# Kernel optimization log

Hardware: AMD Instinct MI355X
Metric: run time of the kernel (lower is better)

## Reference

```python
import jax, jax.numpy as jnp
import numpy as np

TOP_K = 8


def setup_inputs() -> dict:
    key = jax.random.key(0)
    k1, k2 = jax.random.split(key)
    N, D, E = 16384, 4096, 64
    x = jax.random.normal(k1, (N, D), dtype=jnp.float32)
    W = jax.random.normal(k2, (E, D), dtype=jnp.float32) * (1.0 / np.sqrt(D))
    b = jnp.zeros((E,), dtype=jnp.float32)
    return {"x": x, "W": W, "b": b}


def reference(x, W, b):
    # gate: [N, E]
    logits = jnp.einsum('nd,ed->ne', x, W) + b
    top_vals, top_idx = jax.lax.top_k(logits, TOP_K)  # [N, k]
    N = logits.shape[0]
    rows = jnp.arange(N)[:, None]  # [N, 1] broadcast against [N, k]
    neg_inf = jnp.full_like(logits, -jnp.inf)
    sparse = neg_inf.at[rows, top_idx].set(top_vals)
    sparse_logits = jax.nn.softmax(sparse, axis=-1)  # non-topk entries -> 0
    return (sparse_logits, top_idx)
```

## Files before the change

### kernel.cpp

```cpp
#include <hip/hip_runtime.h>
#include <cfloat>
#include <cmath>

#define M     16384
#define K     4096
#define E     64
#define TOPK  8
#define GAP_THRESH 1e-4f

#define SPLIT 4
#define KPS   (K / SPLIT)
#define NCH   (KPS / 32)

typedef __attribute__((ext_vector_type(8))) short bf16x8;
typedef __attribute__((ext_vector_type(4))) float f32x4;


__device__ __forceinline__ short f2bf(float f) {
    unsigned u = __builtin_bit_cast(unsigned, f);
    u += 0x7FFFu + ((u >> 16) & 1u);
    return (short)(u >> 16);
}
__device__ __forceinline__ float bf2f(short h) {
    unsigned u = ((unsigned)(unsigned short)h) << 16;
    return __builtin_bit_cast(float, u);
}

__global__ __launch_bounds__(256) void prep_kernel(const float* __restrict__ W,
                                                   short* __restrict__ Whf,
                                                   short* __restrict__ Wlf,
                                                   int* __restrict__ count) {
    int t = blockIdx.x * 256 + threadIdx.x;
    float w = W[t];
    short h = f2bf(w);
    short lo = f2bf(w - bf2f(h));
    int e = t >> 12, k = t & 4095;
    int gc = k >> 5, kk = k & 31;
    size_t fidx = (((size_t)gc * 4 + (e >> 4)) * 64 + (kk >> 3) * 16 + (e & 15)) * 8
                  + (kk & 7);
    Whf[fidx] = h;
    Wlf[fidx] = lo;
    if (t == 0) *count = 0;
}

struct XW {
    float4 xa, xb;
    bf16x8 h0, h1, h2, h3, l0, l1, l2, l3;
};

__device__ __forceinline__ void load_set(XW& s, const float* gx,
                                         const short* ph, const short* pl, int cc) {
    const int ko = cc * 32;
    s.xa = *reinterpret_cast<const float4*>(gx + ko);
    s.xb = *reinterpret_cast<const float4*>(gx + ko + 4);
    const short* bh = ph + (size_t)cc * 2048;
    const short* bl = pl + (size_t)cc * 2048;
    s.h0 = *reinterpret_cast<const bf16x8*>(bh);
    s.h1 = *reinterpret_cast<const bf16x8*>(bh + 512);
    s.h2 = *reinterpret_cast<const bf16x8*>(bh + 1024);
    s.h3 = *reinterpret_cast<const bf16x8*>(bh + 1536);
    s.l0 = *reinterpret_cast<const bf16x8*>(bl);
    s.l1 = *reinterpret_cast<const bf16x8*>(bl + 512);
    s.l2 = *reinterpret_cast<const bf16x8*>(bl + 1024);
    s.l3 = *reinterpret_cast<const bf16x8*>(bl + 1536);
}

__device__ __forceinline__ void compute_set(const XW& s, f32x4 acc[4]) {
    float vv[8] = {s.xa.x, s.xa.y, s.xa.z, s.xa.w, s.xb.x, s.xb.y, s.xb.z, s.xb.w};
    bf16x8 ah, al;
#pragma unroll
    for (int j = 0; j < 8; ++j) {
        short hh = f2bf(vv[j]);
        ah[j] = hh;
        al[j] = f2bf(vv[j] - bf2f(hh));
    }
    acc[0] = __builtin_amdgcn_mfma_f32_16x16x32_bf16(ah, s.h0, acc[0], 0, 0, 0);
    acc[0] = __builtin_amdgcn_mfma_f32_16x16x32_bf16(ah, s.l0, acc[0], 0, 0, 0);
    acc[0] = __builtin_amdgcn_mfma_f32_16x16x32_bf16(al, s.h0, acc[0], 0, 0, 0);
    acc[1] = __builtin_amdgcn_mfma_f32_16x16x32_bf16(ah, s.h1, acc[1], 0, 0, 0);
    acc[1] = __builtin_amdgcn_mfma_f32_16x16x32_bf16(ah, s.l1, acc[1], 0, 0, 0);
    acc[1] = __builtin_amdgcn_mfma_f32_16x16x32_bf16(al, s.h1, acc[1], 0, 0, 0);
    acc[2] = __builtin_amdgcn_mfma_f32_16x16x32_bf16(ah, s.h2, acc[2], 0, 0, 0);
    acc[2] = __builtin_amdgcn_mfma_f32_16x16x32_bf16(ah, s.l2, acc[2], 0, 0, 0);
    acc[2] = __builtin_amdgcn_mfma_f32_16x16x32_bf16(al, s.h2, acc[2], 0, 0, 0);
    acc[3] = __builtin_amdgcn_mfma_f32_16x16x32_bf16(ah, s.h3, acc[3], 0, 0, 0);
    acc[3] = __builtin_amdgcn_mfma_f32_16x16x32_bf16(ah, s.l3, acc[3], 0, 0, 0);
    acc[3] = __builtin_amdgcn_mfma_f32_16x16x32_bf16(al, s.h3, acc[3], 0, 0, 0);
}

__global__ __launch_bounds__(256) void gate_kernel(
    const float* __restrict__ x,
    const short* __restrict__ Whf,
    const short* __restrict__ Wlf,
    float* __restrict__ part)
{
    const int t  = threadIdx.x;
    const int l  = t & 63;
    const int wv = t >> 6;
    const int h    = blockIdx.x & (SPLIT - 1);
    const int row0 = (blockIdx.x >> 2) * 64 + wv * 16;
    const int k0   = h * KPS;

    const int kg   = l >> 4;
    const int xrow = row0 + (l & 15);

    const float* gx = x + (size_t)xrow * K + k0 + kg * 8;
    const short* ph = Whf + ((size_t)(k0 >> 5) * 4) * 512 + (size_t)l * 8;
    const short* pl = Wlf + ((size_t)(k0 >> 5) * 4) * 512 + (size_t)l * 8;

    f32x4 acc[4] = {{0,0,0,0},{0,0,0,0},{0,0,0,0},{0,0,0,0}};

    XW A, B;
    load_set(A, gx, ph, pl, 0);
    for (int c = 0; c < NCH; c += 2) {
        load_set(B, gx, ph, pl, c + 1);
        compute_set(A, acc);
        if (c + 2 < NCH) load_set(A, gx, ph, pl, c + 2);
        compute_set(B, acc);
    }

#pragma unroll
    for (int et = 0; et < 4; ++et)
#pragma unroll
        for (int r = 0; r < 4; ++r)
            part[((size_t)h * M + row0 + (l >> 4) * 4 + r) * E + et * 16 + (l & 15)]
                = acc[et][r];
}

__global__ __launch_bounds__(256) void reduce_kernel(
    const float* __restrict__ part,
    const float* __restrict__ b,
    float* __restrict__ outp,
    float* __restrict__ outi,
    int*   __restrict__ count,
    int*   __restrict__ list)
{
    const int lane = threadIdx.x & 63;
    const int w    = threadIdx.x >> 6;
    const int row  = blockIdx.x * 4 + w;

    float orig = b[lane];
#pragma unroll
    for (int hh = 0; hh < SPLIT; ++hh)
        orig += part[((size_t)hh * M + row) * E + lane];

    float cur = orig;
    float vals[9];
    float myidxf = 0.0f;
    bool  sel = false;

#pragma unroll
    for (int i = 0; i < 9; ++i) {
        float m = cur;
#pragma unroll
        for (int off = 32; off > 0; off >>= 1)
            m = fmaxf(m, __shfl_xor(m, off, 64));
        unsigned long long msk = __ballot(cur == m);
        int il = __ffsll((long long)msk) - 1;
        vals[i] = m;
        if (lane == il) { cur = -FLT_MAX; if (i < TOPK) sel = true; }
        if (i < TOPK && lane == i) myidxf = (float)il;
    }

    float ssum = 0.0f;
#pragma unroll
    for (int i = 0; i < TOPK; ++i) ssum += expf(vals[i] - vals[0]);
    float p = sel ? (expf(orig - vals[0]) / ssum) : 0.0f;

    outp[(size_t)row * E + lane] = p;
    if (lane < TOPK) outi[(size_t)row * TOPK + lane] = myidxf;

    float mingap = FLT_MAX;
#pragma unroll
    for (int i = 0; i < 8; ++i) mingap = fminf(mingap, vals[i] - vals[i + 1]);
    if (lane == 0 && mingap < GAP_THRESH) {
        int pos = atomicAdd(count, 1);
        if (pos < M) list[pos] = row;
    }
}

__global__ __launch_bounds__(512) void fix_kernel(
    const float* __restrict__ x,
    const float* __restrict__ W,
    const float* __restrict__ b,
    float* __restrict__ outp,
    float* __restrict__ outi,
    const int* __restrict__ count,
    const int* __restrict__ list)
{
    __shared__ float  xs[K];
    __shared__ double lsum[E];
    const int t   = threadIdx.x;
    const int l   = t & 63;
    const int wv  = t >> 6;
    const int cnt = *count;

    for (int i = blockIdx.x; i < cnt; i += gridDim.x) {
        const int row = list[i];

        const float4* xr4 = reinterpret_cast<const float4*>(x + (size_t)row * K);
        reinterpret_cast<float4*>(xs)[t]       = xr4[t];
        reinterpret_cast<float4*>(xs)[512 + t] = xr4[512 + t];
        __syncthreads();

        const int e0 = wv * 8;
        double acc[8] = {};
#pragma unroll 4
        for (int j = 0; j < 16; ++j) {
            float4 xv = reinterpret_cast<const float4*>(xs)[l + 64 * j];
#pragma unroll
            for (int e8 = 0; e8 < 8; ++e8) {
                float4 wv4 = reinterpret_cast<const float4*>(
                    W + (size_t)(e0 + e8) * K)[l + 64 * j];
                acc[e8] = fma((double)xv.x, (double)wv4.x, acc[e8]);
                acc[e8] = fma((double)xv.y, (double)wv4.y, acc[e8]);
                acc[e8] = fma((double)xv.z, (double)wv4.z, acc[e8]);
                acc[e8] = fma((double)xv.w, (double)wv4.w, acc[e8]);
            }
        }

#pragma unroll
        for (int e8 = 0; e8 < 8; ++e8) {
            double v = acc[e8];
#pragma unroll
            for (int off = 32; off > 0; off >>= 1)
                v += __shfl_xor(v, off, 64);
            if (l == e8) lsum[e0 + e8] = v;
        }
        __syncthreads();

        if (wv == 0) {
            const double orig = lsum[l] + (double)b[l];
            double cur = orig;

            double vals[TOPK];
            float  myidxf = 0.0f;
            bool   sel = false;

#pragma unroll
            for (int tt = 0; tt < TOPK; ++tt) {
                double m = cur;
#pragma unroll
                for (int off = 32; off > 0; off >>= 1) {
                    double o = __shfl_xor(m, off, 64);
                    m = fmax(m, o);
                }
                unsigned long long msk = __ballot(cur == m);
                int il = __ffsll((long long)msk) - 1;
                vals[tt] = m;
                if (l == il) { cur = -DBL_MAX; sel = true; }
                if (l == tt)  myidxf = (float)il;
            }

            double ssum = 0.0;
#pragma unroll
            for (int tt = 0; tt < TOPK; ++tt) ssum += exp(vals[tt] - vals[0]);
            float p = sel ? (float)(exp(orig - vals[0]) / ssum) : 0.0f;

            outp[(size_t)row * E + l] = p;
            if (l < TOPK) outi[(size_t)row * TOPK + l] = myidxf;
        }
        __syncthreads();
    }
}

__global__ __launch_bounds__(64) void fallback_kernel(
    const float* __restrict__ x,
    const float* __restrict__ W,
    const float* __restrict__ b,
    float* __restrict__ outp,
    float* __restrict__ outi)
{
    const int row = blockIdx.x * 64 + threadIdx.x;
    double lg[64];
#pragma unroll
    for (int e = 0; e < 64; ++e) lg[e] = (double)b[e];
    const float* xr = x + (size_t)row * K;
    for (int k = 0; k < K; k += 4) {
        float4 xa = *reinterpret_cast<const float4*>(xr + k);
        double xd[4] = {(double)xa.x, (double)xa.y, (double)xa.z, (double)xa.w};
#pragma unroll
        for (int e = 0; e < 64; ++e) {
            const float* wp = W + (size_t)e * K + k;
            double a = lg[e];
#pragma unroll
            for (int j = 0; j < 4; ++j) a = fma(xd[j], (double)wp[j], a);
            lg[e] = a;
        }
    }
    unsigned long long selm = 0ull;
    double vals[TOPK]; int idx[TOPK];
#pragma unroll
    for (int i = 0; i < TOPK; ++i) {
        double m = -DBL_MAX; int mi = 0;
#pragma unroll
        for (int e = 0; e < 64; ++e) {
            bool gt = !((selm >> e) & 1ull) && (lg[e] > m);
            m = gt ? lg[e] : m; mi = gt ? e : mi;
        }
        vals[i] = m; idx[i] = mi; selm |= (1ull << mi);
    }
    double ssum = 0.0;
#pragma unroll
    for (int i = 0; i < TOPK; ++i) ssum += exp(vals[i] - vals[0]);
    double inv = 1.0 / ssum;
#pragma unroll
    for (int e = 0; e < 64; ++e)
        outp[(size_t)row * E + e] =
            ((selm >> e) & 1ull) ? (float)(exp(lg[e] - vals[0]) * inv) : 0.0f;
#pragma unroll
    for (int i = 0; i < TOPK; ++i)
        outi[(size_t)row * TOPK + i] = (float)idx[i];
}

extern "C" void kernel_launch(void* const* d_in, const int* in_sizes, int n_in,
                              void* d_out, int out_size, void* d_ws, size_t ws_size,
                              hipStream_t stream) {
    (void)in_sizes; (void)n_in; (void)out_size;
    const float* x = (const float*)d_in[0];
    const float* W = (const float*)d_in[1];
    const float* b = (const float*)d_in[2];

    float* outp = (float*)d_out;
    float* outi = outp + (size_t)M * E;

    const size_t wh_off   = 0;
    const size_t wl_off   = wh_off + sizeof(short) * (size_t)E * K;
    const size_t cnt_off  = wl_off + sizeof(short) * (size_t)E * K;
    const size_t list_off = cnt_off + 256;
    const size_t part_off = list_off + (size_t)M * sizeof(int);
    const size_t need     = part_off + (size_t)SPLIT * M * E * sizeof(float);

    if (ws_size >= need) {
        short*  Whf  = (short*)((char*)d_ws + wh_off);
        short*  Wlf  = (short*)((char*)d_ws + wl_off);
        int*    cnt  = (int*)((char*)d_ws + cnt_off);
        int*    list = (int*)((char*)d_ws + list_off);
        float*  part = (float*)((char*)d_ws + part_off);

        prep_kernel<<<(E * K) / 256, 256, 0, stream>>>(W, Whf, Wlf, cnt);
        gate_kernel<<<(M / 64) * SPLIT, 256, 0, stream>>>(x, Whf, Wlf, part);
        reduce_kernel<<<M / 4, 256, 0, stream>>>(part, b, outp, outi, cnt, list);
        fix_kernel<<<1024, 512, 0, stream>>>(x, W, b, outp, outi, cnt, list);
    } else {
        fallback_kernel<<<M / 64, 64, 0, stream>>>(x, W, b, outp, outi);
    }
}
```

Before: 128.7 us.

## Fuse near-tie fp64 recompute into reduce kernel, drop fix kernel and atomics

The separate fix kernel, the atomic counter and the row list are removed. Rows whose top-k gap falls below the threshold are now recomputed in fp64 inside the reduce kernel by the same block. This saves a kernel launch, the atomic and the list traffic. In exchange the reduce kernel gains 16KB of shared memory plus more registers, which can lower occupancy for every row, and flagged rows serialize work inside their block.

After: 203.1 us. 1.58x slower.

```diff
diff --git a/kernel.cpp b/kernel.cpp
--- a/kernel.cpp
+++ b/kernel.cpp
@@ -28,8 +28,7 @@
 
 __global__ __launch_bounds__(256) void prep_kernel(const float* __restrict__ W,
                                                    short* __restrict__ Whf,
-                                                   short* __restrict__ Wlf,
-                                                   int* __restrict__ count) {
+                                                   short* __restrict__ Wlf) {
     int t = blockIdx.x * 256 + threadIdx.x;
     float w = W[t];
     short h = f2bf(w);
@@ -40,7 +39,6 @@
                   + (kk & 7);
     Whf[fidx] = h;
     Wlf[fidx] = lo;
-    if (t == 0) *count = 0;
 }
 
 struct XW {
@@ -129,20 +127,25 @@
 
 __global__ __launch_bounds__(256) void reduce_kernel(
     const float* __restrict__ part,
+    const float* __restrict__ x,
+    const float* __restrict__ W,
     const float* __restrict__ b,
     float* __restrict__ outp,
-    float* __restrict__ outi,
-    int*   __restrict__ count,
-    int*   __restrict__ list)
+    float* __restrict__ outi)
 {
-    const int lane = threadIdx.x & 63;
-    const int w    = threadIdx.x >> 6;
-    const int row  = blockIdx.x * 4 + w;
-
-    float orig = b[lane];
+    __shared__ float  xs[K];
+    __shared__ double lsum[E];
+    __shared__ int    rflag[4];
+
+    const int t = threadIdx.x;
+    const int l = t & 63;
+    const int w = t >> 6;
+    const int row = blockIdx.x * 4 + w;
+
+    float orig = b[l];
 #pragma unroll
     for (int hh = 0; hh < SPLIT; ++hh)
-        orig += part[((size_t)hh * M + row) * E + lane];
+        orig += part[((size_t)hh * M + row) * E + l];
 
     float cur = orig;
     float vals[9];
@@ -158,107 +161,87 @@
         unsigned long long msk = __ballot(cur == m);
         int il = __ffsll((long long)msk) - 1;
         vals[i] = m;
-        if (lane == il) { cur = -FLT_MAX; if (i < TOPK) sel = true; }
-        if (i < TOPK && lane == i) myidxf = (float)il;
-    }
-
-    float ssum = 0.0f;
-#pragma unroll
-    for (int i = 0; i < TOPK; ++i) ssum += expf(vals[i] - vals[0]);
-    float p = sel ? (expf(orig - vals[0]) / ssum) : 0.0f;
-
-    outp[(size_t)row * E + lane] = p;
-    if (lane < TOPK) outi[(size_t)row * TOPK + lane] = myidxf;
+        if (l == il) { cur = -FLT_MAX; if (i < TOPK) sel = true; }
+        if (i < TOPK && l == i) myidxf = (float)il;
+    }
 
     float mingap = FLT_MAX;
 #pragma unroll
     for (int i = 0; i < 8; ++i) mingap = fminf(mingap, vals[i] - vals[i + 1]);
-    if (lane == 0 && mingap < GAP_THRESH) {
-        int pos = atomicAdd(count, 1);
-        if (pos < M) list[pos] = row;
-    }
-}
-
-__global__ __launch_bounds__(512) void fix_kernel(
-    const float* __restrict__ x,
-    const float* __restrict__ W,
-    const float* __restrict__ b,
-    float* __restrict__ outp,
-    float* __restrict__ outi,
-    const int* __restrict__ count,
-    const int* __restrict__ list)
-{
-    __shared__ float  xs[K];
-    __shared__ double lsum[E];
-    const int t   = threadIdx.x;
-    const int l   = t & 63;
-    const int wv  = t >> 6;
-    const int cnt = *count;
-
-    for (int i = blockIdx.x; i < cnt; i += gridDim.x) {
-        const int row = list[i];
-
-        const float4* xr4 = reinterpret_cast<const float4*>(x + (size_t)row * K);
-        reinterpret_cast<float4*>(xs)[t]       = xr4[t];
-        reinterpret_cast<float4*>(xs)[512 + t] = xr4[512 + t];
+    const bool flagged = (mingap < GAP_THRESH);
+
+    if (!flagged) {
+        float ssum = 0.0f;
+#pragma unroll
+        for (int i = 0; i < TOPK; ++i) ssum += expf(vals[i] - vals[0]);
+        float p = sel ? (expf(orig - vals[0]) / ssum) : 0.0f;
+        outp[(size_t)row * E + l] = p;
+        if (l < TOPK) outi[(size_t)row * TOPK + l] = myidxf;
+    }
+    if (l == 0) rflag[w] = flagged ? 1 : 0;
+    __syncthreads();
+
+#pragma unroll 1
+    for (int r = 0; r < 4; ++r) {
+        if (rflag[r] == 0) continue;
+        const int rrow = blockIdx.x * 4 + r;
+
+        const float4* xr4 = reinterpret_cast<const float4*>(x + (size_t)rrow * K);
+#pragma unroll
+        for (int j = 0; j < 4; ++j)
+            reinterpret_cast<float4*>(xs)[j * 256 + t] = xr4[j * 256 + t];
         __syncthreads();
 
-        const int e0 = wv * 8;
-        double acc[8] = {};
-#pragma unroll 4
-        for (int j = 0; j < 16; ++j) {
-            float4 xv = reinterpret_cast<const float4*>(xs)[l + 64 * j];
-#pragma unroll
-            for (int e8 = 0; e8 < 8; ++e8) {
-                float4 wv4 = reinterpret_cast<const float4*>(
-                    W + (size_t)(e0 + e8) * K)[l + 64 * j];
-                acc[e8] = fma((double)xv.x, (double)wv4.x, acc[e8]);
-                acc[e8] = fma((double)xv.y, (double)wv4.y, acc[e8]);
-                acc[e8] = fma((double)xv.z, (double)wv4.z, acc[e8]);
-                acc[e8] = fma((double)xv.w, (double)wv4.w, acc[e8]);
+#pragma unroll 2
+        for (int ei = 0; ei < 16; ++ei) {
+            const int e = w * 16 + ei;
+            const float4* wr = reinterpret_cast<const float4*>(W + (size_t)e * K);
+            double s = 0.0;
+#pragma unroll
+            for (int j = 0; j < 16; ++j) {
+                float4 wv4 = wr[l + 64 * j];
+                float4 xv  = reinterpret_cast<const float4*>(xs)[l + 64 * j];
+                s = fma((double)xv.x, (double)wv4.x, s);
+                s = fma((double)xv.y, (double)wv4.y, s);
+                s = fma((double)xv.z, (double)wv4.z, s);
+                s = fma((double)xv.w, (double)wv4.w, s);
             }
-        }
-
-#pragma unroll
-        for (int e8 = 0; e8 < 8; ++e8) {
-            double v = acc[e8];
 #pragma unroll
             for (int off = 32; off > 0; off >>= 1)
-                v += __shfl_xor(v, off, 64);
-            if (l == e8) lsum[e0 + e8] = v;
+                s += __shfl_xor(s, off, 64);
+            if (l == 0) lsum[e] = s;
         }
         __syncthreads();
 
-        if (wv == 0) {
-            const double orig = lsum[l] + (double)b[l];
-            double cur = orig;
-
-            double vals[TOPK];
-            float  myidxf = 0.0f;
-            bool   sel = false;
+        if (w == r) {
+            const double origd = lsum[l] + (double)b[l];
+            double curd = origd;
+            double dvals[TOPK];
+            float  midx = 0.0f;
+            bool   dsel = false;
 
 #pragma unroll
             for (int tt = 0; tt < TOPK; ++tt) {
-                double m = cur;
+                double m = curd;
 #pragma unroll
                 for (int off = 32; off > 0; off >>= 1) {
                     double o = __shfl_xor(m, off, 64);
                     m = fmax(m, o);
                 }
-                unsigned long long msk = __ballot(cur == m);
+                unsigned long long msk = __ballot(curd == m);
                 int il = __ffsll((long long)msk) - 1;
-                vals[tt] = m;
-                if (l == il) { cur = -DBL_MAX; sel = true; }
-                if (l == tt)  myidxf = (float)il;
+                dvals[tt] = m;
+                if (l == il) { curd = -DBL_MAX; dsel = true; }
+                if (l == tt)  midx = (float)il;
             }
 
             double ssum = 0.0;
 #pragma unroll
-            for (int tt = 0; tt < TOPK; ++tt) ssum += exp(vals[tt] - vals[0]);
-            float p = sel ? (float)(exp(orig - vals[0]) / ssum) : 0.0f;
-
-            outp[(size_t)row * E + l] = p;
-            if (l < TOPK) outi[(size_t)row * TOPK + l] = myidxf;
+            for (int tt = 0; tt < TOPK; ++tt) ssum += exp(dvals[tt] - dvals[0]);
+            float p = dsel ? (float)(exp(origd - dvals[0]) / ssum) : 0.0f;
+
+            outp[(size_t)rrow * E + l] = p;
+            if (l < TOPK) outi[(size_t)rrow * TOPK + l] = midx;
         }
         __syncthreads();
     }
@@ -326,22 +309,17 @@
 
     const size_t wh_off   = 0;
     const size_t wl_off   = wh_off + sizeof(short) * (size_t)E * K;
-    const size_t cnt_off  = wl_off + sizeof(short) * (size_t)E * K;
-    const size_t list_off = cnt_off + 256;
-    const size_t part_off = list_off + (size_t)M * sizeof(int);
+    const size_t part_off = wl_off + sizeof(short) * (size_t)E * K;
     const size_t need     = part_off + (size_t)SPLIT * M * E * sizeof(float);
 
     if (ws_size >= need) {
         short*  Whf  = (short*)((char*)d_ws + wh_off);
         short*  Wlf  = (short*)((char*)d_ws + wl_off);
-        int*    cnt  = (int*)((char*)d_ws + cnt_off);
-        int*    list = (int*)((char*)d_ws + list_off);
         float*  part = (float*)((char*)d_ws + part_off);
 
-        prep_kernel<<<(E * K) / 256, 256, 0, stream>>>(W, Whf, Wlf, cnt);
+        prep_kernel<<<(E * K) / 256, 256, 0, stream>>>(W, Whf, Wlf);
         gate_kernel<<<(M / 64) * SPLIT, 256, 0, stream>>>(x, Whf, Wlf, part);
-        reduce_kernel<<<M / 4, 256, 0, stream>>>(part, b, outp, outi, cnt, list);
-        fix_kernel<<<1024, 512, 0, stream>>>(x, W, b, outp, outi, cnt, list);
+        reduce_kernel<<<M / 4, 256, 0, stream>>>(part, x, W, b, outp, outi);
     } else {
         fallback_kernel<<<M / 64, 64, 0, stream>>>(x, W, b, outp, outi);
     }
```

## Split fp64 fix-up pass into K-sliced partial-sum kernel plus reduce/top-k kernel

Applied to the files above, without the earlier changes.

Replaces the single fix kernel, where one block computes all 64 fp64 logits for a flagged row, with two kernels. The first spreads each flagged row across eight 512-wide K slices, writing fp64 partial sums to workspace. The second sums the partials, then runs top-k and softmax. This raises parallelism for the small set of near-tie rows, at the cost of an extra launch and a workspace round trip. The flagged-row count is now capped at RCAP=2048, so rows beyond that would be left uncorrected.

New measurement: 127.3 us. Within noise of the previous version (-1.1%).

```diff
diff --git a/kernel.cpp b/kernel.cpp
--- a/kernel.cpp
+++ b/kernel.cpp
@@ -11,6 +11,8 @@
 #define SPLIT 4
 #define KPS   (K / SPLIT)
 #define NCH   (KPS / 32)
+#define RCAP  2048
+#define FKS   8
 
 typedef __attribute__((ext_vector_type(8))) short bf16x8;
 typedef __attribute__((ext_vector_type(4))) float f32x4;
@@ -179,88 +181,121 @@
     }
 }
 
-__global__ __launch_bounds__(512) void fix_kernel(
+__global__ __launch_bounds__(256) void fix1_kernel(
     const float* __restrict__ x,
     const float* __restrict__ W,
-    const float* __restrict__ b,
+    double* __restrict__ dsum,
+    const int* __restrict__ count,
+    const int* __restrict__ list)
+{
+    __shared__ float xsl[512];
+    const int t   = threadIdx.x;
+    const int l   = t & 63;
+    const int wv  = t >> 6;
+    const int tot = min(*count, RCAP) * FKS;
+
+    for (int p = blockIdx.x; p < tot; p += gridDim.x) {
+        const int i   = p >> 3;
+        const int ks  = p & 7;
+        const int row = list[i];
+        const int k0  = ks << 9;
+
+        if (t < 128)
+            reinterpret_cast<float4*>(xsl)[t] =
+                reinterpret_cast<const float4*>(x + (size_t)row * K + k0)[t];
+        __syncthreads();
+
+        const float4* xs4 = reinterpret_cast<const float4*>(xsl);
+
+#pragma unroll
+        for (int g = 0; g < 2; ++g) {
+            const int e0 = wv * 16 + g * 8;
+            float4 w0[8], w1[8];
+#pragma unroll
+            for (int e8 = 0; e8 < 8; ++e8) {
+                const float4* wp = reinterpret_cast<const float4*>(
+                    W + (size_t)(e0 + e8) * K + k0);
+                w0[e8] = wp[l];
+                w1[e8] = wp[l + 64];
+            }
+            float4 xv0 = xs4[l];
+            float4 xv1 = xs4[l + 64];
+
+            double s[8];
+#pragma unroll
+            for (int e8 = 0; e8 < 8; ++e8) {
+                double a = 0.0;
+                a = fma((double)xv0.x, (double)w0[e8].x, a);
+                a = fma((double)xv0.y, (double)w0[e8].y, a);
+                a = fma((double)xv0.z, (double)w0[e8].z, a);
+                a = fma((double)xv0.w, (double)w0[e8].w, a);
+                a = fma((double)xv1.x, (double)w1[e8].x, a);
+                a = fma((double)xv1.y, (double)w1[e8].y, a);
+                a = fma((double)xv1.z, (double)w1[e8].z, a);
+                a = fma((double)xv1.w, (double)w1[e8].w, a);
+                s[e8] = a;
+            }
+
+#pragma unroll
+            for (int e8 = 0; e8 < 8; ++e8) {
+                double v = s[e8];
+#pragma unroll
+                for (int off = 32; off > 0; off >>= 1)
+                    v += __shfl_xor(v, off, 64);
+                if (l == 0)
+                    dsum[((size_t)i * FKS + ks) * E + e0 + e8] = v;
+            }
+        }
+        __syncthreads();
+    }
+}
+
+__global__ __launch_bounds__(64) void fix2_kernel(
+    const double* __restrict__ dsum,
+    const float*  __restrict__ b,
     float* __restrict__ outp,
     float* __restrict__ outi,
     const int* __restrict__ count,
     const int* __restrict__ list)
 {
-    __shared__ float  xs[K];
-    __shared__ double lsum[E];
-    const int t   = threadIdx.x;
-    const int l   = t & 63;
-    const int wv  = t >> 6;
-    const int cnt = *count;
+    const int l   = threadIdx.x;
+    const int cnt = min(*count, RCAP);
 
     for (int i = blockIdx.x; i < cnt; i += gridDim.x) {
         const int row = list[i];
 
-        const float4* xr4 = reinterpret_cast<const float4*>(x + (size_t)row * K);
-        reinterpret_cast<float4*>(xs)[t]       = xr4[t];
-        reinterpret_cast<float4*>(xs)[512 + t] = xr4[512 + t];
-        __syncthreads();
-
-        const int e0 = wv * 8;
-        double acc[8] = {};
-#pragma unroll 4
-        for (int j = 0; j < 16; ++j) {
-            float4 xv = reinterpret_cast<const float4*>(xs)[l + 64 * j];
-#pragma unroll
-            for (int e8 = 0; e8 < 8; ++e8) {
-                float4 wv4 = reinterpret_cast<const float4*>(
-                    W + (size_t)(e0 + e8) * K)[l + 64 * j];
-                acc[e8] = fma((double)xv.x, (double)wv4.x, acc[e8]);
-                acc[e8] = fma((double)xv.y, (double)wv4.y, acc[e8]);
-                acc[e8] = fma((double)xv.z, (double)wv4.z, acc[e8]);
-                acc[e8] = fma((double)xv.w, (double)wv4.w, acc[e8]);
+        double orig = (double)b[l];
+#pragma unroll
+        for (int ks = 0; ks < FKS; ++ks)
+            orig += dsum[((size_t)i * FKS + ks) * E + l];
+
+        double cur = orig;
+        double vals[TOPK];
+        float  myidxf = 0.0f;
+        bool   sel = false;
+
+#pragma unroll
+        for (int tt = 0; tt < TOPK; ++tt) {
+            double m = cur;
+#pragma unroll
+            for (int off = 32; off > 0; off >>= 1) {
+                double o = __shfl_xor(m, off, 64);
+                m = fmax(m, o);
             }
+            unsigned long long msk = __ballot(cur == m);
+            int il = __ffsll((long long)msk) - 1;
+            vals[tt] = m;
+            if (l == il) { cur = -DBL_MAX; sel = true; }
+            if (l == tt)  myidxf = (float)il;
         }
 
-#pragma unroll
-        for (int e8 = 0; e8 < 8; ++e8) {
-            double v = acc[e8];
-#pragma unroll
-            for (int off = 32; off > 0; off >>= 1)
-                v += __shfl_xor(v, off, 64);
-            if (l == e8) lsum[e0 + e8] = v;
-        }
-        __syncthreads();
-
-        if (wv == 0) {
-            const double orig = lsum[l] + (double)b[l];
-            double cur = orig;
-
-            double vals[TOPK];
-            float  myidxf = 0.0f;
-            bool   sel = false;
-
-#pragma unroll
-            for (int tt = 0; tt < TOPK; ++tt) {
-                double m = cur;
-#pragma unroll
-                for (int off = 32; off > 0; off >>= 1) {
-                    double o = __shfl_xor(m, off, 64);
-                    m = fmax(m, o);
-                }
-                unsigned long long msk = __ballot(cur == m);
-                int il = __ffsll((long long)msk) - 1;
-                vals[tt] = m;
-                if (l == il) { cur = -DBL_MAX; sel = true; }
-                if (l == tt)  myidxf = (float)il;
-            }
-
-            double ssum = 0.0;
-#pragma unroll
-            for (int tt = 0; tt < TOPK; ++tt) ssum += exp(vals[tt] - vals[0]);
-            float p = sel ? (float)(exp(orig - vals[0]) / ssum) : 0.0f;
-
-            outp[(size_t)row * E + l] = p;
-            if (l < TOPK) outi[(size_t)row * TOPK + l] = myidxf;
-        }
-        __syncthreads();
+        double ssum = 0.0;
+#pragma unroll
+        for (int tt = 0; tt < TOPK; ++tt) ssum += exp(vals[tt] - vals[0]);
+        float p = sel ? (float)(exp(orig - vals[0]) / ssum) : 0.0f;
+
+        outp[(size_t)row * E + l] = p;
+        if (l < TOPK) outi[(size_t)row * TOPK + l] = myidxf;
     }
 }
 
@@ -329,7 +364,8 @@
     const size_t cnt_off  = wl_off + sizeof(short) * (size_t)E * K;
     const size_t list_off = cnt_off + 256;
     const size_t part_off = list_off + (size_t)M * sizeof(int);
-    const size_t need     = part_off + (size_t)SPLIT * M * E * sizeof(float);
+    const size_t dsum_off = part_off + (size_t)SPLIT * M * E * sizeof(float);
+    const size_t need     = dsum_off + (size_t)RCAP * FKS * E * sizeof(double);
 
     if (ws_size >= need) {
         short*  Whf  = (short*)((char*)d_ws + wh_off);
@@ -337,11 +373,13 @@
         int*    cnt  = (int*)((char*)d_ws + cnt_off);
         int*    list = (int*)((char*)d_ws + list_off);
         float*  part = (float*)((char*)d_ws + part_off);
+        double* dsum = (double*)((char*)d_ws + dsum_off);
 
         prep_kernel<<<(E * K) / 256, 256, 0, stream>>>(W, Whf, Wlf, cnt);
         gate_kernel<<<(M / 64) * SPLIT, 256, 0, stream>>>(x, Whf, Wlf, part);
         reduce_kernel<<<M / 4, 256, 0, stream>>>(part, b, outp, outi, cnt, list);
-        fix_kernel<<<1024, 512, 0, stream>>>(x, W, b, outp, outi, cnt, list);
+        fix1_kernel<<<4096, 256, 0, stream>>>(x, W, dsum, cnt, list);
+        fix2_kernel<<<1024, 64, 0, stream>>>(dsum, b, outp, outi, cnt, list);
     } else {
         fallback_kernel<<<M / 64, 64, 0, stream>>>(x, W, b, outp, outi);
     }
```
